# Optimization experiments

Measured on AMD Instinct MI355X. Metric: run time of the kernel, lower is better.

Reference implementation:

```python
import jax, jax.numpy as jnp
import numpy as np

N, E, D, H, ED = 50000, 800000, 64, 8, 16
DH = D // H  # 8


def setup_inputs() -> dict:
    key = jax.random.key(0)
    ks = jax.random.split(key, 16)
    s = 0.05
    return {
        "x": jax.random.normal(ks[0], (N, D), jnp.float32),
        "edge_index": jax.random.randint(ks[1], (2, E), 0, N, jnp.int32),
        "edge_attr": jax.random.normal(ks[2], (E, ED), jnp.float32),
        "Wq": jax.random.normal(ks[3], (D, D), jnp.float32) * s,
        "bq": jnp.zeros((D,), jnp.float32),
        "Wk": jax.random.normal(ks[4], (D, D), jnp.float32) * s,
        "bk": jnp.zeros((D,), jnp.float32),
        "Wv": jax.random.normal(ks[5], (D, D), jnp.float32) * s,
        "bv": jnp.zeros((D,), jnp.float32),
        "We": jax.random.normal(ks[6], (ED, D), jnp.float32) * s,
        "be": jnp.zeros((D,), jnp.float32),
        "Wskip": jax.random.normal(ks[7], (D, D), jnp.float32) * s,
        "bskip": jnp.zeros((D,), jnp.float32),
        "Wbeta": jax.random.normal(ks[8], (3 * D, 1), jnp.float32) * s,
        "gamma": jnp.ones((D,), jnp.float32),
        "beta_bn": jnp.zeros((D,), jnp.float32),
    }


def reference(x, edge_index, edge_attr, Wq, bq, Wk, bk, Wv, bv, We, be,
              Wskip, bskip, Wbeta, gamma, beta_bn):
    n, d = x.shape
    src, dst = edge_index[0], edge_index[1]
    # per-node projections, then gather per edge (PyG TransformerConv)
    q = (x @ Wq + bq).reshape(n, H, DH)
    k = (x @ Wk + bk).reshape(n, H, DH)
    v = (x @ Wv + bv).reshape(n, H, DH)
    e = (edge_attr @ We + be).reshape(-1, H, DH)
    ke = k[src] + e                      # [E,H,DH]
    ve = v[src] + e                      # [E,H,DH]
    logits = (q[dst] * ke).sum(-1) / jnp.sqrt(jnp.float32(DH))  # [E,H]
    # segment softmax over incoming edges of each destination node
    m = jax.ops.segment_max(logits, dst, num_segments=n)
    p = jnp.exp(logits - m[dst])
    denom = jax.ops.segment_sum(p, dst, num_segments=n)
    alpha = p / (denom[dst] + 1e-16)     # [E,H]
    out = jax.ops.segment_sum(alpha[:, :, None] * ve, dst, num_segments=n)
    out = out.reshape(n, d)              # concat heads
    # beta-gated skip connection (beta=True, root_weight=True)
    x_r = x @ Wskip + bskip
    g = jax.nn.sigmoid(jnp.concatenate([out, x_r, out - x_r], axis=-1) @ Wbeta)
    out = g * x_r + (1.0 - g) * out
    # BatchNorm1d (training forward: batch statistics), eps=1e-5
    mean = out.mean(axis=0)
    var = out.var(axis=0)
    out = (out - mean) * jax.lax.rsqrt(var + 1e-5) * gamma + beta_bn
    # LeakyReLU(0.01); dropout is identity in eval
    return jnp.where(out >= 0, out, 0.01 * out)
```

## Files before the change

### kernel.cpp

```cpp
#include <hip/hip_runtime.h>

#define D   64
#define H   8
#define DH  8
#define ED  16
#define QK_SCALE 0.35355339059327373f

typedef unsigned int uint_t;
typedef __attribute__((ext_vector_type(8))) short bf16x8;
typedef __attribute__((ext_vector_type(4))) float f32x4;

__device__ __forceinline__ void fma4(float4& a, float s, const float4& w) {
    a.x += s * w.x; a.y += s * w.y; a.z += s * w.z; a.w += s * w.w;
}
__device__ __forceinline__ uint_t f2bf(float f) {
    uint_t u = __float_as_uint(f);
    return (u + 0x7FFFu + ((u >> 16) & 1u)) >> 16;
}
__device__ __forceinline__ float bf_lo(uint_t u) { return __uint_as_float(u << 16); }
__device__ __forceinline__ float bf_hi(uint_t u) { return __uint_as_float(u & 0xFFFF0000u); }

__device__ __forceinline__ float khreduce8(const float* acc, int e) {
    int b0 = e & 1, b1 = (e >> 1) & 1, b2 = (e >> 2) & 1;
    float t0[4];
    #pragma unroll
    for (int j = 0; j < 4; ++j) {
        float k = b0 ? acc[2*j+1] : acc[2*j];
        float s = b0 ? acc[2*j]   : acc[2*j+1];
        t0[j] = k + __shfl_xor(s, 8);
    }
    float t1[2];
    #pragma unroll
    for (int j = 0; j < 2; ++j) {
        float k = b1 ? t0[2*j+1] : t0[2*j];
        float s = b1 ? t0[2*j]   : t0[2*j+1];
        t1[j] = k + __shfl_xor(s, 16);
    }
    float k = b2 ? t1[1] : t1[0];
    float s = b2 ? t1[0] : t1[1];
    return k + __shfl_xor(s, 32);
}

__global__ __launch_bounds__(256) void proj_qs_hist(
    const float* __restrict__ x,
    const float* __restrict__ Wq, const float* __restrict__ bq,
    const float* __restrict__ Ws, const float* __restrict__ bs,
    const float* __restrict__ We, const float* __restrict__ be,
    uint_t* __restrict__ qxr,
    uint_t* __restrict__ Ap, float* __restrict__ qbe, int N,
    const int* __restrict__ ei, int* __restrict__ cnt, int E, int projBlocks)
{
    __shared__ float sW[2][D * D];
    __shared__ float sWe[ED * D];
    __shared__ float sbe[D];
    if (blockIdx.x >= projBlocks) {
        int gid = (blockIdx.x - projBlocks) * 256 + threadIdx.x;
        if (gid < E) atomicAdd(&cnt[ei[E + gid]], 1);
        return;
    }
    {
        for (int t = threadIdx.x; t < D * D; t += 256) {
            sW[0][t] = Wq[t];
            sW[1][t] = Ws[t];
        }
        for (int t = threadIdx.x; t < ED * D; t += 256) sWe[t] = We[t];
        if (threadIdx.x < D) sbe[threadIdx.x] = be[threadIdx.x];
    }
    __syncthreads();

    int cg = (threadIdx.x & 15) * 4;
    float4 vbq = *(const float4*)(bq + cg);
    float4 vbs = *(const float4*)(bs + cg);
    int h  = cg >> 3;
    int hh = (cg >> 2) & 1;

    #pragma unroll 1
    for (int it = 0; it < 4; ++it) {
        int node = blockIdx.x * 64 + it * 16 + (threadIdx.x >> 4);
        if (node >= N) return;

        float4 aq = {0,0,0,0}, as_ = {0,0,0,0};
        const float* xrow = x + (size_t)node * D;

        #pragma unroll
        for (int i = 0; i < D; i += 4) {
            float4 xv = *(const float4*)(xrow + i);
            #pragma unroll
            for (int s = 0; s < 4; ++s) {
                float xs = (&xv.x)[s];
                fma4(aq,  xs, *(const float4*)(&sW[0][(i + s) * D + cg]));
                fma4(as_, xs, *(const float4*)(&sW[1][(i + s) * D + cg]));
            }
        }
        aq.x = (aq.x + vbq.x) * QK_SCALE;
        aq.y = (aq.y + vbq.y) * QK_SCALE;
        aq.z = (aq.z + vbq.z) * QK_SCALE;
        aq.w = (aq.w + vbq.w) * QK_SCALE;
        as_.x += vbs.x; as_.y += vbs.y; as_.z += vbs.z; as_.w += vbs.w;

        uint4 pqx;
        pqx.x = f2bf(aq.x) | (f2bf(as_.x) << 16);
        pqx.y = f2bf(aq.y) | (f2bf(as_.y) << 16);
        pqx.z = f2bf(aq.z) | (f2bf(as_.z) << 16);
        pqx.w = f2bf(aq.w) | (f2bf(as_.w) << 16);
        *(uint4*)(qxr + (size_t)node * D + cg) = pqx;

        float part[ED];
        #pragma unroll
        for (int i = 0; i < ED; ++i) {
            float4 we4 = *(const float4*)(&sWe[i * D + cg]);
            part[i] = aq.x * we4.x + aq.y * we4.y + aq.z * we4.z + aq.w * we4.w;
        }
        float4 be4 = *(const float4*)(&sbe[cg]);
        float qb = aq.x * be4.x + aq.y * be4.y + aq.z * be4.z + aq.w * be4.w;
        #pragma unroll
        for (int i = 0; i < ED; ++i) part[i] += __shfl_xor(part[i], 1);
        qb += __shfl_xor(qb, 1);

        uint4 apk;
        apk.x = f2bf(part[hh * 8 + 0]) | (f2bf(part[hh * 8 + 1]) << 16);
        apk.y = f2bf(part[hh * 8 + 2]) | (f2bf(part[hh * 8 + 3]) << 16);
        apk.z = f2bf(part[hh * 8 + 4]) | (f2bf(part[hh * 8 + 5]) << 16);
        apk.w = f2bf(part[hh * 8 + 6]) | (f2bf(part[hh * 8 + 7]) << 16);
        *(uint4*)(Ap + (size_t)node * 64 + h * 8 + hh * 4) = apk;
        if (hh == 0) qbe[(size_t)node * 8 + h] = qb;
    }
}

__global__ __launch_bounds__(256) void proj_kv_scana(
    const float* __restrict__ x,
    const float* __restrict__ Wk, const float* __restrict__ bk,
    const float* __restrict__ Wv, const float* __restrict__ bv,
    uint_t* __restrict__ kvp, int N, int kvBlocks,
    const int* __restrict__ cnt, int* __restrict__ bsum)
{
    __shared__ int red[256];
    if (blockIdx.x >= kvBlocks) {
        int t = threadIdx.x;
        int i = (blockIdx.x - kvBlocks) * 256 + t;
        red[t] = (i < N) ? cnt[i] : 0;
        __syncthreads();
        for (int s = 128; s > 0; s >>= 1) {
            if (t < s) red[t] += red[t + s];
            __syncthreads();
        }
        if (t == 0) bsum[blockIdx.x - kvBlocks] = red[0];
        return;
    }

    int lane = threadIdx.x & 63;
    int wv   = threadIdx.x >> 6;
    int l = lane & 15, g = lane >> 4;

    bf16x8 Bf[2][4][2];
    #pragma unroll
    for (int ct = 0; ct < 4; ++ct)
        #pragma unroll
        for (int kh = 0; kh < 2; ++kh)
            #pragma unroll
            for (int j = 0; j < 8; ++j) {
                int k = kh * 32 + g * 8 + j;
                int c = ct * 16 + l;
                Bf[0][ct][kh][j] = (short)f2bf(Wk[k * 64 + c]);
                Bf[1][ct][kh][j] = (short)f2bf(Wv[k * 64 + c]);
            }
    float bkc[4], bvc[4];
    #pragma unroll
    for (int ct = 0; ct < 4; ++ct) {
        bkc[ct] = bk[ct * 16 + l];
        bvc[ct] = bv[ct * 16 + l];
    }

    int nt   = (N + 15) >> 4;
    int wtot = kvBlocks * 4;
    for (int t = blockIdx.x * 4 + wv; t < nt; t += wtot) {
        int n0 = t * 16;
        bf16x8 Af[2];
        const float* xr = x + (size_t)(n0 + l) * 64 + g * 8;
        #pragma unroll
        for (int kh = 0; kh < 2; ++kh) {
            float4 p0 = *(const float4*)(xr + kh * 32);
            float4 p1 = *(const float4*)(xr + kh * 32 + 4);
            Af[kh][0] = (short)f2bf(p0.x); Af[kh][1] = (short)f2bf(p0.y);
            Af[kh][2] = (short)f2bf(p0.z); Af[kh][3] = (short)f2bf(p0.w);
            Af[kh][4] = (short)f2bf(p1.x); Af[kh][5] = (short)f2bf(p1.y);
            Af[kh][6] = (short)f2bf(p1.z); Af[kh][7] = (short)f2bf(p1.w);
        }
        #pragma unroll
        for (int ct = 0; ct < 4; ++ct) {
            f32x4 ck = {0.f, 0.f, 0.f, 0.f};
            f32x4 cv = {0.f, 0.f, 0.f, 0.f};
            ck = __builtin_amdgcn_mfma_f32_16x16x32_bf16(Af[0], Bf[0][ct][0], ck, 0, 0, 0);
            ck = __builtin_amdgcn_mfma_f32_16x16x32_bf16(Af[1], Bf[0][ct][1], ck, 0, 0, 0);
            cv = __builtin_amdgcn_mfma_f32_16x16x32_bf16(Af[0], Bf[1][ct][0], cv, 0, 0, 0);
            cv = __builtin_amdgcn_mfma_f32_16x16x32_bf16(Af[1], Bf[1][ct][1], cv, 0, 0, 0);
            #pragma unroll
            for (int r = 0; r < 4; ++r) {
                int node = n0 + g * 4 + r;
                uint_t pk = f2bf(ck[r] + bkc[ct]) | (f2bf(cv[r] + bvc[ct]) << 16);
                kvp[(size_t)node * 64 + ct * 16 + l] = pk;
            }
        }
    }
}

__global__ __launch_bounds__(256) void scan_c(
    const int* __restrict__ cnt, const int* __restrict__ bsum,
    int* __restrict__ row_start, int* __restrict__ cursor, int N, int E, int nb)
{
    __shared__ int sb[256];
    __shared__ int sh[256];
    int t = threadIdx.x;
    int bv = (t < nb) ? bsum[t] : 0;
    sb[t] = bv;
    __syncthreads();
    for (int s = 1; s < 256; s <<= 1) {
        int a = (t >= s) ? sb[t - s] : 0;
        __syncthreads();
        sb[t] += a;
        __syncthreads();
    }
    int boff = sb[blockIdx.x] - bsum[blockIdx.x];

    int i = blockIdx.x * 256 + t;
    int v = (i < N) ? cnt[i] : 0;
    sh[t] = v;
    __syncthreads();
    for (int s = 1; s < 256; s <<= 1) {
        int a = (t >= s) ? sh[t - s] : 0;
        __syncthreads();
        sh[t] += a;
        __syncthreads();
    }
    int excl = sh[t] - v + boff;
    if (i < N) { row_start[i] = excl; cursor[i] = excl; }
    if (i == N - 1) row_start[N] = E;
}

__global__ __launch_bounds__(256) void csr_scatter(
    const int* __restrict__ ei, const float4* __restrict__ ea4,
    int* __restrict__ cursor, int* __restrict__ srcs_s,
    uint_t* __restrict__ ea_s, int E)
{
    int gid = blockIdx.x * 256 + threadIdx.x;
    if (gid >= E) return;
    int src = ei[gid];
    int dst = ei[E + gid];
    float4 r0 = ea4[(size_t)gid * 4 + 0];
    float4 r1 = ea4[(size_t)gid * 4 + 1];
    float4 r2 = ea4[(size_t)gid * 4 + 2];
    float4 r3 = ea4[(size_t)gid * 4 + 3];
    int pos = atomicAdd(&cursor[dst], 1);
    srcs_s[pos] = src;
    uint4 p0, p1;
    p0.x = f2bf(r0.x) | (f2bf(r0.y) << 16);
    p0.y = f2bf(r0.z) | (f2bf(r0.w) << 16);
    p0.z = f2bf(r1.x) | (f2bf(r1.y) << 16);
    p0.w = f2bf(r1.z) | (f2bf(r1.w) << 16);
    p1.x = f2bf(r2.x) | (f2bf(r2.y) << 16);
    p1.y = f2bf(r2.z) | (f2bf(r2.w) << 16);
    p1.z = f2bf(r3.x) | (f2bf(r3.y) << 16);
    p1.w = f2bf(r3.z) | (f2bf(r3.w) << 16);
    *(uint4*)(ea_s + (size_t)pos * 8)     = p0;
    *(uint4*)(ea_s + (size_t)pos * 8 + 4) = p1;
}

__global__ __launch_bounds__(256, 4) void node_gather(
    const int*   __restrict__ row_start,
    const int*   __restrict__ srcs_s,
    const uint_t* __restrict__ ea_s,
    const float* __restrict__ We, const float* __restrict__ be,
    const uint_t* __restrict__ qxr, const uint_t* __restrict__ kvp,
    const uint_t* __restrict__ Ap, const float* __restrict__ qbe,
    const float* __restrict__ Wbeta,
    float* __restrict__ out, float* __restrict__ S1p, float* __restrict__ S2p,
    int N)
{
    __shared__ float l1[4][D];
    __shared__ float l2[4][D];
    int lane = threadIdx.x & 63;
    int w    = threadIdx.x >> 6;
    int h    = lane & 7;
    int e    = lane >> 3;
    int cmix = h * 8 + e;

    float w0[8], w1[8];
    #pragma unroll
    for (int j = 0; j < 8; ++j) {
        w0[j] = We[(2 * e)     * D + h * 8 + j];
        w1[j] = We[(2 * e + 1) * D + h * 8 + j];
    }
    float bev = be[cmix];
    float wb0 = Wbeta[cmix], wb1 = Wbeta[D + cmix], wb2 = Wbeta[2 * D + cmix];

    float s1bn = 0.f, s2bn = 0.f;
    int stride = gridDim.x * 4;

    for (int nid = blockIdx.x * 4 + w; nid < N; nid += stride) {
        int rs  = row_start[nid];
        int deg = row_start[nid + 1] - rs;

        const uint4* qxp = (const uint4*)(qxr + (size_t)nid * D + h * 8);
        uint4 qx0 = qxp[0], qx1 = qxp[1];
        float q8[8];
        q8[0] = bf_lo(qx0.x); q8[1] = bf_lo(qx0.y);
        q8[2] = bf_lo(qx0.z); q8[3] = bf_lo(qx0.w);
        q8[4] = bf_lo(qx1.x); q8[5] = bf_lo(qx1.y);
        q8[6] = bf_lo(qx1.z); q8[7] = bf_lo(qx1.w);
        uint_t xru0 = (e & 2) ? ((e & 1) ? qx0.w : qx0.z)
                              : ((e & 1) ? qx0.y : qx0.x);
        uint_t xru1 = (e & 2) ? ((e & 1) ? qx1.w : qx1.z)
                              : ((e & 1) ? qx1.y : qx1.x);
        float xrv = bf_hi((e & 4) ? xru1 : xru0);

        const uint4* app = (const uint4*)(Ap + (size_t)nid * 64 + h * 8);
        uint4 au0 = app[0], au1 = app[1];
        float a16[ED];
        #pragma unroll
        for (int j = 0; j < 4; ++j) {
            a16[j * 2]         = bf_lo((&au0.x)[j]);
            a16[j * 2 + 1]     = bf_hi((&au0.x)[j]);
            a16[8 + j * 2]     = bf_lo((&au1.x)[j]);
            a16[8 + j * 2 + 1] = bf_hi((&au1.x)[j]);
        }
        float qbeh = qbe[(size_t)nid * 8 + h];

        float acc[8] = {0,0,0,0,0,0,0,0};
        float sv[ED] = {0,0,0,0,0,0,0,0,0,0,0,0,0,0,0,0};
        float den = 0.f;

        int src_next = (e < deg) ? srcs_s[rs + e] : 0;

        for (int j0 = 0; j0 < deg; j0 += 8) {
            int src = src_next;
            {
                int enx = j0 + 8 + e;
                src_next = (enx < deg) ? srcs_s[rs + enx] : 0;
            }
            int eidx = j0 + e;
            bool valid = eidx < deg;
            int ce = valid ? eidx : 0;

            const uint4* kp = (const uint4*)(kvp + (size_t)src * 64 + h * 8);
            uint4 k0 = kp[0], k1 = kp[1];
            const uint4* ep = (const uint4*)(ea_s + (size_t)(rs + ce) * 8);
            uint4 u0 = ep[0], u1 = ep[1];

            float ex[ED];
            #pragma unroll
            for (int j = 0; j < 4; ++j) {
                ex[j * 2]         = bf_lo((&u0.x)[j]);
                ex[j * 2 + 1]     = bf_hi((&u0.x)[j]);
                ex[8 + j * 2]     = bf_lo((&u1.x)[j]);
                ex[8 + j * 2 + 1] = bf_hi((&u1.x)[j]);
            }
            float c = qbeh;
            c += q8[0] * bf_lo(k0.x); c += q8[1] * bf_lo(k0.y);
            c += q8[2] * bf_lo(k0.z); c += q8[3] * bf_lo(k0.w);
            c += q8[4] * bf_lo(k1.x); c += q8[5] * bf_lo(k1.y);
            c += q8[6] * bf_lo(k1.z); c += q8[7] * bf_lo(k1.w);
            #pragma unroll
            for (int i = 0; i < ED; ++i) c += ex[i] * a16[i];

            float p = valid ? __expf(c) : 0.f;
            den += p;
            acc[0] += p * bf_hi(k0.x); acc[1] += p * bf_hi(k0.y);
            acc[2] += p * bf_hi(k0.z); acc[3] += p * bf_hi(k0.w);
            acc[4] += p * bf_hi(k1.x); acc[5] += p * bf_hi(k1.y);
            acc[6] += p * bf_hi(k1.z); acc[7] += p * bf_hi(k1.w);
            #pragma unroll
            for (int i = 0; i < ED; ++i) sv[i] += p * ex[i];
        }

        den += __shfl_xor(den, 8);
        den += __shfl_xor(den, 16);
        den += __shfl_xor(den, 32);

        float u[8];
        #pragma unroll
        for (int j = 0; j < 8; ++j) {
            int i0 = ((j & 6) << 1) | (j & 1);
            float k = (e & 1) ? sv[i0 | 2] : sv[i0];
            float s = (e & 1) ? sv[i0] : sv[i0 | 2];
            u[j] = k + __shfl_xor(s, 8);
        }
        float v2[4];
        #pragma unroll
        for (int j = 0; j < 4; ++j) {
            int j0 = ((j & 2) << 1) | (j & 1);
            float k = (e & 2) ? u[j0 | 2] : u[j0];
            float s = (e & 2) ? u[j0] : u[j0 | 2];
            v2[j] = k + __shfl_xor(s, 16);
        }
        float S0, S1;
        {
            float k0 = (e & 4) ? v2[2] : v2[0];
            float s0 = (e & 4) ? v2[0] : v2[2];
            S0 = k0 + __shfl_xor(s0, 32);
            float k1 = (e & 4) ? v2[3] : v2[1];
            float s1 = (e & 4) ? v2[1] : v2[3];
            S1 = k1 + __shfl_xor(s1, 32);
        }

        float cj[8];
        #pragma unroll
        for (int j = 0; j < 8; ++j) cj[j] = S0 * w0[j] + S1 * w1[j];
        float esum = khreduce8(cj, e);
        float vsum = khreduce8(acc, e);

        float o = (vsum + esum + bev * den) / (den + 1e-16f);

        float tb  = o * wb0 + xrv * wb1 + (o - xrv) * wb2;
        #pragma unroll
        for (int s = 1; s < 64; s <<= 1) tb += __shfl_xor(tb, s);
        float g  = 1.f / (1.f + __expf(-tb));
        float o2 = g * xrv + (1.f - g) * o;
        out[(size_t)nid * D + cmix] = o2;
        s1bn += o2; s2bn += o2 * o2;
    }

    l1[w][cmix] = s1bn; l2[w][cmix] = s2bn;
    __syncthreads();
    if (threadIdx.x < D) {
        float a = l1[0][threadIdx.x] + l1[1][threadIdx.x]
                + l1[2][threadIdx.x] + l1[3][threadIdx.x];
        float b = l2[0][threadIdx.x] + l2[1][threadIdx.x]
                + l2[2][threadIdx.x] + l2[3][threadIdx.x];
        unsafeAtomicAdd(&S1p[threadIdx.x * 64], a);
        unsafeAtomicAdd(&S2p[threadIdx.x * 64], b);
    }
}

__global__ __launch_bounds__(256) void bn_apply(
    float4* __restrict__ out, const float* __restrict__ S1p,
    const float* __restrict__ S2p, const float* __restrict__ gamma,
    const float* __restrict__ beta, int total4, float invN)
{
    int gid = blockIdx.x * 256 + threadIdx.x;
    if (gid >= total4) return;
    int col = (gid & 15) * 4;
    float4 g4 = *(const float4*)(gamma + col);
    float4 b4 = *(const float4*)(beta + col);
    float4 y  = out[gid];
    #pragma unroll
    for (int j = 0; j < 4; ++j) {
        float mean = S1p[(col + j) * 64] * invN;
        float var  = S2p[(col + j) * 64] * invN - mean * mean;
        float sc   = (&g4.x)[j] * rsqrtf(var + 1e-5f);
        float sh   = (&b4.x)[j] - mean * sc;
        float tv   = (&y.x)[j] * sc + sh;
        (&y.x)[j]  = (tv >= 0.f) ? tv : 0.01f * tv;
    }
    out[gid] = y;
}

extern "C" void kernel_launch(void* const* d_in, const int* in_sizes, int n_in,
                              void* d_out, int out_size, void* d_ws, size_t ws_size,
                              hipStream_t stream)
{
    const float* x     = (const float*)d_in[0];
    const int*   ei    = (const int*)  d_in[1];
    const float* ea    = (const float*)d_in[2];
    const float* Wq    = (const float*)d_in[3];
    const float* bq    = (const float*)d_in[4];
    const float* Wk    = (const float*)d_in[5];
    const float* bk    = (const float*)d_in[6];
    const float* Wv    = (const float*)d_in[7];
    const float* bv    = (const float*)d_in[8];
    const float* We    = (const float*)d_in[9];
    const float* be    = (const float*)d_in[10];
    const float* Wskip = (const float*)d_in[11];
    const float* bskip = (const float*)d_in[12];
    const float* Wbeta = (const float*)d_in[13];
    const float* gamma = (const float*)d_in[14];
    const float* betab = (const float*)d_in[15];

    int N = in_sizes[0] / D;
    int E = in_sizes[1] / 2;

    int*    ws        = (int*)d_ws;
    int*    cnt       = ws;
    float*  S1p       = (float*)(ws + 50000);
    float*  S2p       = (float*)(ws + 54096);
    int*    row_start = ws + 58192;
    int*    bsum      = ws + 108240;
    int*    srcs_s    = ws + 108544;
    uint_t* ea_s      = (uint_t*)(ws + 908544);
    uint_t* kvp       = (uint_t*)(ws + 7308544);
    uint_t* qxr       = (uint_t*)(ws + 10508544);
    uint_t* Ap        = (uint_t*)(ws + 13708544);
    float*  qbe       = (float*)(ws + 16908544);

    hipMemsetAsync(d_ws, 0, (size_t)58192 * sizeof(int), stream);

    int projB = (N + 63) / 64;
    int histB = (E + 255) / 256;
    proj_qs_hist<<<projB + histB, 256, 0, stream>>>(
        x, Wq, bq, Wskip, bskip, We, be,
        qxr, Ap, qbe, N, ei, cnt, E, projB);

    int scanB = (N + 255) / 256;
    int kvB   = 196;
    proj_kv_scana<<<kvB + scanB, 256, 0, stream>>>(
        x, Wk, bk, Wv, bv, kvp, N, kvB, cnt, bsum);

    scan_c<<<scanB, 256, 0, stream>>>(cnt, bsum, row_start, cnt, N, E, scanB);

    csr_scatter<<<(E + 255) / 256, 256, 0, stream>>>(
        ei, (const float4*)ea, cnt, srcs_s, ea_s, E);

    node_gather<<<1024, 256, 0, stream>>>(
        row_start, srcs_s, ea_s, We, be, qxr, kvp, Ap, qbe, Wbeta,
        (float*)d_out, S1p, S2p, N);

    bn_apply<<<(N * 16 + 255) / 256, 256, 0, stream>>>(
        (float4*)d_out, S1p, S2p, gamma, betab, N * 16, 1.0f / (float)N);
}
```

Measured before the change: 189.9 us.

## Fold Wq·We into a combined weight and compute edge-attention projections via MFMA

Precomputes combined weight matrices WA = Wq·We^T per head (and Wq·be, bq·We, bq·be) in an extra block of the first kernel. The per-node Ap and qbe values are then computed directly from x with bf16 MFMA in the kv projection kernel, rather than through scalar FMA and shuffles after the q projection. The point is to take the shared-memory We work and shuffles out of the q/skip projection kernel and run it on matrix cores. In exchange the kv kernel holds more register fragments, Ap is rounded to bf16 from a different product order, and correctness depends on the first kernel finishing before the second on the same stream.

Measured after the change: 212.6 us. 11.9% more time.

```diff
diff --git a/kernel.cpp b/kernel.cpp
--- a/kernel.cpp
+++ b/kernel.cpp
@@ -7,6 +7,7 @@
 #define QK_SCALE 0.35355339059327373f
 
 typedef unsigned int uint_t;
+typedef unsigned short ushort_t;
 typedef __attribute__((ext_vector_type(8))) short bf16x8;
 typedef __attribute__((ext_vector_type(4))) float f32x4;
 
@@ -46,37 +47,66 @@
     const float* __restrict__ Wq, const float* __restrict__ bq,
     const float* __restrict__ Ws, const float* __restrict__ bs,
     const float* __restrict__ We, const float* __restrict__ be,
-    uint_t* __restrict__ qxr,
-    uint_t* __restrict__ Ap, float* __restrict__ qbe, int N,
-    const int* __restrict__ ei, int* __restrict__ cnt, int E, int projBlocks)
+    uint_t* __restrict__ qxr, int N,
+    const int* __restrict__ ei, int* __restrict__ cnt, int E,
+    float* __restrict__ WA, float* __restrict__ Abias,
+    float* __restrict__ Wqbe, float* __restrict__ qbeb,
+    int histB, int projB)
 {
     __shared__ float sW[2][D * D];
-    __shared__ float sWe[ED * D];
-    __shared__ float sbe[D];
-    if (blockIdx.x >= projBlocks) {
-        int gid = (blockIdx.x - projBlocks) * 256 + threadIdx.x;
+    if (blockIdx.x < histB) {
+        int gid = blockIdx.x * 256 + threadIdx.x;
         if (gid < E) atomicAdd(&cnt[ei[E + gid]], 1);
         return;
     }
-    {
-        for (int t = threadIdx.x; t < D * D; t += 256) {
-            sW[0][t] = Wq[t];
-            sW[1][t] = Ws[t];
-        }
-        for (int t = threadIdx.x; t < ED * D; t += 256) sWe[t] = We[t];
-        if (threadIdx.x < D) sbe[threadIdx.x] = be[threadIdx.x];
+    if (blockIdx.x >= histB + projB) {
+        for (int idx = threadIdx.x; idx < 64 * 128; idx += 256) {
+            int k = idx >> 7, c = idx & 127, h = c >> 4, i = c & 15;
+            float s = 0.f;
+            #pragma unroll
+            for (int dh = 0; dh < 8; ++dh)
+                s += Wq[k * 64 + h * 8 + dh] * We[i * 64 + h * 8 + dh];
+            WA[idx] = s * QK_SCALE;
+        }
+        for (int idx = threadIdx.x; idx < 64 * 8; idx += 256) {
+            int k = idx >> 3, h = idx & 7;
+            float s = 0.f;
+            #pragma unroll
+            for (int dh = 0; dh < 8; ++dh)
+                s += Wq[k * 64 + h * 8 + dh] * be[h * 8 + dh];
+            Wqbe[idx] = s * QK_SCALE;
+        }
+        if (threadIdx.x < 128) {
+            int h = threadIdx.x >> 4, i = threadIdx.x & 15;
+            float s = 0.f;
+            #pragma unroll
+            for (int dh = 0; dh < 8; ++dh)
+                s += bq[h * 8 + dh] * We[i * 64 + h * 8 + dh];
+            Abias[threadIdx.x] = s * QK_SCALE;
+        }
+        if (threadIdx.x < 8) {
+            float s = 0.f;
+            #pragma unroll
+            for (int dh = 0; dh < 8; ++dh)
+                s += bq[threadIdx.x * 8 + dh] * be[threadIdx.x * 8 + dh];
+            qbeb[threadIdx.x] = s * QK_SCALE;
+        }
+        return;
+    }
+    int pb = blockIdx.x - histB;
+    for (int t = threadIdx.x; t < D * D; t += 256) {
+        sW[0][t] = Wq[t];
+        sW[1][t] = Ws[t];
     }
     __syncthreads();
 
     int cg = (threadIdx.x & 15) * 4;
     float4 vbq = *(const float4*)(bq + cg);
     float4 vbs = *(const float4*)(bs + cg);
-    int h  = cg >> 3;
-    int hh = (cg >> 2) & 1;
 
     #pragma unroll 1
     for (int it = 0; it < 4; ++it) {
-        int node = blockIdx.x * 64 + it * 16 + (threadIdx.x >> 4);
+        int node = pb * 64 + it * 16 + (threadIdx.x >> 4);
         if (node >= N) return;
 
         float4 aq = {0,0,0,0}, as_ = {0,0,0,0};
@@ -104,26 +134,6 @@
         pqx.z = f2bf(aq.z) | (f2bf(as_.z) << 16);
         pqx.w = f2bf(aq.w) | (f2bf(as_.w) << 16);
         *(uint4*)(qxr + (size_t)node * D + cg) = pqx;
-
-        float part[ED];
-        #pragma unroll
-        for (int i = 0; i < ED; ++i) {
-            float4 we4 = *(const float4*)(&sWe[i * D + cg]);
-            part[i] = aq.x * we4.x + aq.y * we4.y + aq.z * we4.z + aq.w * we4.w;
-        }
-        float4 be4 = *(const float4*)(&sbe[cg]);
-        float qb = aq.x * be4.x + aq.y * be4.y + aq.z * be4.z + aq.w * be4.w;
-        #pragma unroll
-        for (int i = 0; i < ED; ++i) part[i] += __shfl_xor(part[i], 1);
-        qb += __shfl_xor(qb, 1);
-
-        uint4 apk;
-        apk.x = f2bf(part[hh * 8 + 0]) | (f2bf(part[hh * 8 + 1]) << 16);
-        apk.y = f2bf(part[hh * 8 + 2]) | (f2bf(part[hh * 8 + 3]) << 16);
-        apk.z = f2bf(part[hh * 8 + 4]) | (f2bf(part[hh * 8 + 5]) << 16);
-        apk.w = f2bf(part[hh * 8 + 6]) | (f2bf(part[hh * 8 + 7]) << 16);
-        *(uint4*)(Ap + (size_t)node * 64 + h * 8 + hh * 4) = apk;
-        if (hh == 0) qbe[(size_t)node * 8 + h] = qb;
     }
 }
 
@@ -131,7 +141,10 @@
     const float* __restrict__ x,
     const float* __restrict__ Wk, const float* __restrict__ bk,
     const float* __restrict__ Wv, const float* __restrict__ bv,
-    uint_t* __restrict__ kvp, int N, int kvBlocks,
+    const float* __restrict__ WA, const float* __restrict__ Abias,
+    const float* __restrict__ Wqbe, const float* __restrict__ qbeb,
+    uint_t* __restrict__ kvp, uint_t* __restrict__ Ap,
+    float* __restrict__ qbe, int N, int kvBlocks,
     const int* __restrict__ cnt, int* __restrict__ bsum)
 {
     __shared__ int red[256];
@@ -164,15 +177,37 @@
                 Bf[0][ct][kh][j] = (short)f2bf(Wk[k * 64 + c]);
                 Bf[1][ct][kh][j] = (short)f2bf(Wv[k * 64 + c]);
             }
-    float bkc[4], bvc[4];
+    bf16x8 BA[8][2];
+    #pragma unroll
+    for (int ct = 0; ct < 8; ++ct)
+        #pragma unroll
+        for (int kh = 0; kh < 2; ++kh)
+            #pragma unroll
+            for (int j = 0; j < 8; ++j)
+                BA[ct][kh][j] = (short)f2bf(WA[(kh * 32 + g * 8 + j) * 128 + ct * 16 + l]);
+    bf16x8 Bqb[2];
+    #pragma unroll
+    for (int kh = 0; kh < 2; ++kh)
+        #pragma unroll
+        for (int j = 0; j < 8; ++j)
+            Bqb[kh][j] = (l < 8) ? (short)f2bf(Wqbe[(kh * 32 + g * 8 + j) * 8 + l])
+                                 : (short)0;
+
+    float bkc[4], bvc[4], abl[8];
     #pragma unroll
     for (int ct = 0; ct < 4; ++ct) {
         bkc[ct] = bk[ct * 16 + l];
         bvc[ct] = bv[ct * 16 + l];
     }
+    #pragma unroll
+    for (int ct = 0; ct < 8; ++ct) abl[ct] = Abias[ct * 16 + l];
+    float qbl = (l < 8) ? qbeb[l] : 0.f;
+
+    ushort_t* Ap_us = (ushort_t*)Ap;
 
     int nt   = (N + 15) >> 4;
     int wtot = kvBlocks * 4;
+    #pragma unroll 1
     for (int t = blockIdx.x * 4 + wv; t < nt; t += wtot) {
         int n0 = t * 16;
         bf16x8 Af[2];
@@ -199,6 +234,28 @@
                 int node = n0 + g * 4 + r;
                 uint_t pk = f2bf(ck[r] + bkc[ct]) | (f2bf(cv[r] + bvc[ct]) << 16);
                 kvp[(size_t)node * 64 + ct * 16 + l] = pk;
+            }
+        }
+        #pragma unroll
+        for (int ct = 0; ct < 8; ++ct) {
+            f32x4 ca = {0.f, 0.f, 0.f, 0.f};
+            ca = __builtin_amdgcn_mfma_f32_16x16x32_bf16(Af[0], BA[ct][0], ca, 0, 0, 0);
+            ca = __builtin_amdgcn_mfma_f32_16x16x32_bf16(Af[1], BA[ct][1], ca, 0, 0, 0);
+            #pragma unroll
+            for (int r = 0; r < 4; ++r) {
+                int node = n0 + g * 4 + r;
+                Ap_us[(size_t)node * 128 + ct * 16 + l] =
+                    (ushort_t)f2bf(ca[r] + abl[ct]);
+            }
+        }
+        {
+            f32x4 cq = {0.f, 0.f, 0.f, 0.f};
+            cq = __builtin_amdgcn_mfma_f32_16x16x32_bf16(Af[0], Bqb[0], cq, 0, 0, 0);
+            cq = __builtin_amdgcn_mfma_f32_16x16x32_bf16(Af[1], Bqb[1], cq, 0, 0, 0);
+            if (l < 8) {
+                #pragma unroll
+                for (int r = 0; r < 4; ++r)
+                    qbe[(size_t)(n0 + g * 4 + r) * 8 + l] = cq[r] + qbl;
             }
         }
     }
@@ -490,19 +547,24 @@
     uint_t* qxr       = (uint_t*)(ws + 10508544);
     uint_t* Ap        = (uint_t*)(ws + 13708544);
     float*  qbe       = (float*)(ws + 16908544);
+    float*  WA        = (float*)(ws + 17308544);
+    float*  Abias     = (float*)(ws + 17316736);
+    float*  Wqbe      = (float*)(ws + 17316864);
+    float*  qbeb      = (float*)(ws + 17317376);
 
     hipMemsetAsync(d_ws, 0, (size_t)58192 * sizeof(int), stream);
 
     int projB = (N + 63) / 64;
     int histB = (E + 255) / 256;
-    proj_qs_hist<<<projB + histB, 256, 0, stream>>>(
+    proj_qs_hist<<<histB + projB + 1, 256, 0, stream>>>(
         x, Wq, bq, Wskip, bskip, We, be,
-        qxr, Ap, qbe, N, ei, cnt, E, projB);
+        qxr, N, ei, cnt, E, WA, Abias, Wqbe, qbeb, histB, projB);
 
     int scanB = (N + 255) / 256;
     int kvB   = 196;
     proj_kv_scana<<<kvB + scanB, 256, 0, stream>>>(
-        x, Wk, bk, Wv, bv, kvp, N, kvB, cnt, bsum);
+        x, Wk, bk, Wv, bv, WA, Abias, Wqbe, qbeb,
+        kvp, Ap, qbe, N, kvB, cnt, bsum);
 
     scan_c<<<scanB, 256, 0, stream>>>(cnt, bsum, row_start, cnt, N, E, scanB);
 
```

## Use bf16 MFMA for Q/skip projection and move edge-attr fold to second kernel

Applied to the files above, without the earlier changes.

The Q and skip projections now run on bf16 MFMA instructions in a grid-strided loop of 16-node tiles, mirroring the existing K/V path, in place of scalar FMA from shared memory. The per-node q·We and q·be fold (Ap, qbe) moves into extra blocks of the second kernel, which read the bf16 q values already written to qxr. This cuts the ALU cost and shared-memory traffic of the first kernel. In exchange, x is rounded to bf16 before the matmul and the second kernel gains many one-node-per-wave blocks that each reload We into shared memory.

Result: slower. 213.9 us (+12.6%).

```diff
diff --git a/kernel.cpp b/kernel.cpp
--- a/kernel.cpp
+++ b/kernel.cpp
@@ -10,9 +10,6 @@
 typedef __attribute__((ext_vector_type(8))) short bf16x8;
 typedef __attribute__((ext_vector_type(4))) float f32x4;
 
-__device__ __forceinline__ void fma4(float4& a, float s, const float4& w) {
-    a.x += s * w.x; a.y += s * w.y; a.z += s * w.z; a.w += s * w.w;
-}
 __device__ __forceinline__ uint_t f2bf(float f) {
     uint_t u = __float_as_uint(f);
     return (u + 0x7FFFu + ((u >> 16) & 1u)) >> 16;
@@ -45,85 +42,70 @@
     const float* __restrict__ x,
     const float* __restrict__ Wq, const float* __restrict__ bq,
     const float* __restrict__ Ws, const float* __restrict__ bs,
-    const float* __restrict__ We, const float* __restrict__ be,
-    uint_t* __restrict__ qxr,
-    uint_t* __restrict__ Ap, float* __restrict__ qbe, int N,
-    const int* __restrict__ ei, int* __restrict__ cnt, int E, int projBlocks)
-{
-    __shared__ float sW[2][D * D];
-    __shared__ float sWe[ED * D];
-    __shared__ float sbe[D];
-    if (blockIdx.x >= projBlocks) {
-        int gid = (blockIdx.x - projBlocks) * 256 + threadIdx.x;
+    uint_t* __restrict__ qxr, int N,
+    const int* __restrict__ ei, int* __restrict__ cnt, int E, int histB,
+    int qsBlocks)
+{
+    if (blockIdx.x < histB) {
+        int gid = blockIdx.x * 256 + threadIdx.x;
         if (gid < E) atomicAdd(&cnt[ei[E + gid]], 1);
         return;
     }
-    {
-        for (int t = threadIdx.x; t < D * D; t += 256) {
-            sW[0][t] = Wq[t];
-            sW[1][t] = Ws[t];
-        }
-        for (int t = threadIdx.x; t < ED * D; t += 256) sWe[t] = We[t];
-        if (threadIdx.x < D) sbe[threadIdx.x] = be[threadIdx.x];
-    }
-    __syncthreads();
-
-    int cg = (threadIdx.x & 15) * 4;
-    float4 vbq = *(const float4*)(bq + cg);
-    float4 vbs = *(const float4*)(bs + cg);
-    int h  = cg >> 3;
-    int hh = (cg >> 2) & 1;
-
-    #pragma unroll 1
-    for (int it = 0; it < 4; ++it) {
-        int node = blockIdx.x * 64 + it * 16 + (threadIdx.x >> 4);
-        if (node >= N) return;
-
-        float4 aq = {0,0,0,0}, as_ = {0,0,0,0};
-        const float* xrow = x + (size_t)node * D;
-
-        #pragma unroll
-        for (int i = 0; i < D; i += 4) {
-            float4 xv = *(const float4*)(xrow + i);
-            #pragma unroll
-            for (int s = 0; s < 4; ++s) {
-                float xs = (&xv.x)[s];
-                fma4(aq,  xs, *(const float4*)(&sW[0][(i + s) * D + cg]));
-                fma4(as_, xs, *(const float4*)(&sW[1][(i + s) * D + cg]));
+    int pb   = blockIdx.x - histB;
+    int lane = threadIdx.x & 63;
+    int wv   = threadIdx.x >> 6;
+    int l = lane & 15, g = lane >> 4;
+
+    bf16x8 Bf[2][4][2];
+    #pragma unroll
+    for (int ct = 0; ct < 4; ++ct)
+        #pragma unroll
+        for (int kh = 0; kh < 2; ++kh)
+            #pragma unroll
+            for (int j = 0; j < 8; ++j) {
+                int k = kh * 32 + g * 8 + j;
+                int c = ct * 16 + l;
+                Bf[0][ct][kh][j] = (short)f2bf(Wq[k * 64 + c]);
+                Bf[1][ct][kh][j] = (short)f2bf(Ws[k * 64 + c]);
             }
-        }
-        aq.x = (aq.x + vbq.x) * QK_SCALE;
-        aq.y = (aq.y + vbq.y) * QK_SCALE;
-        aq.z = (aq.z + vbq.z) * QK_SCALE;
-        aq.w = (aq.w + vbq.w) * QK_SCALE;
-        as_.x += vbs.x; as_.y += vbs.y; as_.z += vbs.z; as_.w += vbs.w;
-
-        uint4 pqx;
-        pqx.x = f2bf(aq.x) | (f2bf(as_.x) << 16);
-        pqx.y = f2bf(aq.y) | (f2bf(as_.y) << 16);
-        pqx.z = f2bf(aq.z) | (f2bf(as_.z) << 16);
-        pqx.w = f2bf(aq.w) | (f2bf(as_.w) << 16);
-        *(uint4*)(qxr + (size_t)node * D + cg) = pqx;
-
-        float part[ED];
-        #pragma unroll
-        for (int i = 0; i < ED; ++i) {
-            float4 we4 = *(const float4*)(&sWe[i * D + cg]);
-            part[i] = aq.x * we4.x + aq.y * we4.y + aq.z * we4.z + aq.w * we4.w;
-        }
-        float4 be4 = *(const float4*)(&sbe[cg]);
-        float qb = aq.x * be4.x + aq.y * be4.y + aq.z * be4.z + aq.w * be4.w;
-        #pragma unroll
-        for (int i = 0; i < ED; ++i) part[i] += __shfl_xor(part[i], 1);
-        qb += __shfl_xor(qb, 1);
-
-        uint4 apk;
-        apk.x = f2bf(part[hh * 8 + 0]) | (f2bf(part[hh * 8 + 1]) << 16);
-        apk.y = f2bf(part[hh * 8 + 2]) | (f2bf(part[hh * 8 + 3]) << 16);
-        apk.z = f2bf(part[hh * 8 + 4]) | (f2bf(part[hh * 8 + 5]) << 16);
-        apk.w = f2bf(part[hh * 8 + 6]) | (f2bf(part[hh * 8 + 7]) << 16);
-        *(uint4*)(Ap + (size_t)node * 64 + h * 8 + hh * 4) = apk;
-        if (hh == 0) qbe[(size_t)node * 8 + h] = qb;
+    float bqc[4], bsc[4];
+    #pragma unroll
+    for (int ct = 0; ct < 4; ++ct) {
+        bqc[ct] = bq[ct * 16 + l];
+        bsc[ct] = bs[ct * 16 + l];
+    }
+
+    int nt   = (N + 15) >> 4;
+    int wtot = qsBlocks * 4;
+    for (int t = pb * 4 + wv; t < nt; t += wtot) {
+        int n0 = t * 16;
+        bf16x8 Af[2];
+        const float* xr = x + (size_t)(n0 + l) * 64 + g * 8;
+        #pragma unroll
+        for (int kh = 0; kh < 2; ++kh) {
+            float4 p0 = *(const float4*)(xr + kh * 32);
+            float4 p1 = *(const float4*)(xr + kh * 32 + 4);
+            Af[kh][0] = (short)f2bf(p0.x); Af[kh][1] = (short)f2bf(p0.y);
+            Af[kh][2] = (short)f2bf(p0.z); Af[kh][3] = (short)f2bf(p0.w);
+            Af[kh][4] = (short)f2bf(p1.x); Af[kh][5] = (short)f2bf(p1.y);
+            Af[kh][6] = (short)f2bf(p1.z); Af[kh][7] = (short)f2bf(p1.w);
+        }
+        #pragma unroll
+        for (int ct = 0; ct < 4; ++ct) {
+            f32x4 cq = {0.f, 0.f, 0.f, 0.f};
+            f32x4 cx = {0.f, 0.f, 0.f, 0.f};
+            cq = __builtin_amdgcn_mfma_f32_16x16x32_bf16(Af[0], Bf[0][ct][0], cq, 0, 0, 0);
+            cq = __builtin_amdgcn_mfma_f32_16x16x32_bf16(Af[1], Bf[0][ct][1], cq, 0, 0, 0);
+            cx = __builtin_amdgcn_mfma_f32_16x16x32_bf16(Af[0], Bf[1][ct][0], cx, 0, 0, 0);
+            cx = __builtin_amdgcn_mfma_f32_16x16x32_bf16(Af[1], Bf[1][ct][1], cx, 0, 0, 0);
+            #pragma unroll
+            for (int r = 0; r < 4; ++r) {
+                int node = n0 + g * 4 + r;
+                uint_t pk = f2bf((cq[r] + bqc[ct]) * QK_SCALE)
+                          | (f2bf(cx[r] + bsc[ct]) << 16);
+                qxr[(size_t)node * 64 + ct * 16 + l] = pk;
+            }
+        }
     }
 }
 
@@ -131,11 +113,16 @@
     const float* __restrict__ x,
     const float* __restrict__ Wk, const float* __restrict__ bk,
     const float* __restrict__ Wv, const float* __restrict__ bv,
-    uint_t* __restrict__ kvp, int N, int kvBlocks,
+    const float* __restrict__ We, const float* __restrict__ be,
+    const uint_t* __restrict__ qxr,
+    uint_t* __restrict__ kvp, uint_t* __restrict__ Ap,
+    float* __restrict__ qbe, int N, int kvBlocks, int scanBlocks,
     const int* __restrict__ cnt, int* __restrict__ bsum)
 {
-    __shared__ int red[256];
-    if (blockIdx.x >= kvBlocks) {
+    __shared__ int   red[256];
+    __shared__ float sWe[ED * D];
+    __shared__ float sbe[D];
+    if (blockIdx.x >= kvBlocks && blockIdx.x < kvBlocks + scanBlocks) {
         int t = threadIdx.x;
         int i = (blockIdx.x - kvBlocks) * 256 + t;
         red[t] = (i < N) ? cnt[i] : 0;
@@ -145,6 +132,29 @@
             __syncthreads();
         }
         if (t == 0) bsum[blockIdx.x - kvBlocks] = red[0];
+        return;
+    }
+    if (blockIdx.x >= kvBlocks + scanBlocks) {
+        for (int t = threadIdx.x; t < ED * D; t += 256) sWe[t] = We[t];
+        if (threadIdx.x < D) sbe[threadIdx.x] = be[threadIdx.x];
+        __syncthreads();
+
+        int lane = threadIdx.x & 63;
+        int nid  = (blockIdx.x - kvBlocks - scanBlocks) * 4 + (threadIdx.x >> 6);
+        if (nid >= N) return;
+
+        int h = lane >> 3, t = lane & 7;
+        float qv = bf_lo(qxr[(size_t)nid * 64 + lane]);
+        float a0 = 0.f, a1 = 0.f, qb = 0.f;
+        #pragma unroll
+        for (int dh = 0; dh < 8; ++dh) {
+            float qd = __shfl(qv, (lane & 56) + dh);
+            a0 += qd * sWe[(2 * t)     * D + h * 8 + dh];
+            a1 += qd * sWe[(2 * t + 1) * D + h * 8 + dh];
+            qb += qd * sbe[h * 8 + dh];
+        }
+        Ap[(size_t)nid * 64 + lane] = f2bf(a0) | (f2bf(a1) << 16);
+        if (t == 0) qbe[(size_t)nid * 8 + h] = qb;
         return;
     }
 
@@ -493,16 +503,17 @@
 
     hipMemsetAsync(d_ws, 0, (size_t)58192 * sizeof(int), stream);
 
-    int projB = (N + 63) / 64;
     int histB = (E + 255) / 256;
-    proj_qs_hist<<<projB + histB, 256, 0, stream>>>(
-        x, Wq, bq, Wskip, bskip, We, be,
-        qxr, Ap, qbe, N, ei, cnt, E, projB);
-
-    int scanB = (N + 255) / 256;
-    int kvB   = 196;
-    proj_kv_scana<<<kvB + scanB, 256, 0, stream>>>(
-        x, Wk, bk, Wv, bv, kvp, N, kvB, cnt, bsum);
+    int qsB   = 196;
+    proj_qs_hist<<<histB + qsB, 256, 0, stream>>>(
+        x, Wq, bq, Wskip, bskip, qxr, N, ei, cnt, E, histB, qsB);
+
+    int scanB  = (N + 255) / 256;
+    int kvB    = 196;
+    int aprojB = (N + 3) / 4;
+    proj_kv_scana<<<kvB + scanB + aprojB, 256, 0, stream>>>(
+        x, Wk, bk, Wv, bv, We, be, qxr,
+        kvp, Ap, qbe, N, kvB, scanB, cnt, bsum);
 
     scan_c<<<scanB, 256, 0, stream>>>(cnt, bsum, row_start, cnt, N, E, scanB);
 
```
